# Kernel optimization log

Measured on AMD Instinct MI355X. Metric: run time of the kernel, lower is better.

## Reference

```python
import jax, jax.numpy as jnp
import numpy as np

ALPHA = 0.01  # ema_decay

def setup_inputs() -> dict:
    key = jax.random.key(0)
    k1, k2 = jax.random.split(key)
    B, S, H = 8, 2048, 2048
    x = jax.random.normal(k1, (B, S, H), dtype=jnp.float32)
    W = jax.random.normal(k2, (H, H), dtype=jnp.float32) * (1.0 / np.sqrt(H))
    b = jnp.zeros((H,), dtype=jnp.float32)
    return {"x": x, "W": W, "b": b}

def reference(x, W, b):
    B, S, H = x.shape
    dt = x.dtype
    # p = [S-1, S-2, ..., 0]; w_prime = (1-alpha)^p
    p = jnp.arange(S - 1, -1, -1, dtype=dt)
    one_m_a = jnp.asarray(1.0 - ALPHA, dtype=dt)
    w_prime = one_m_a ** p                                   # [S]
    # w = w_prime, but positions t>=1 scaled by alpha
    w = jnp.where(jnp.arange(S) >= 1, w_prime * ALPHA, w_prime)  # [S]
    c = jnp.cumsum(x * w[None, :, None], axis=1)             # [B,S,H]
    s = c / w_prime[None, :, None]                           # [B,S,H]
    # nn.Linear: s @ W^T + b
    return jnp.einsum('bsh,oh->bso', s, W) + b
```

## Files before the change

### kernel.cpp

```cpp
#include <hip/hip_runtime.h>
#include <cstdint>
#include <cstddef>

#define ALPHA 0.01f
#define A1    0.99f
#define B_    8
#define S_    2048
#define H_    2048
#define NCH   8
#define CL    256
#define NKT   32

typedef __attribute__((ext_vector_type(8))) short bf16x8;
typedef __attribute__((ext_vector_type(4))) float f32x4;

__device__ __forceinline__ unsigned short f2bf(float f) {
    unsigned int u = __float_as_uint(f);
    u += 0x7FFFu + ((u >> 16) & 1u);
    return (unsigned short)(u >> 16);
}

__device__ __forceinline__ void gld16(const void* g, void* l) {
    __builtin_amdgcn_global_load_lds(
        (const __attribute__((address_space(1))) unsigned int*)g,
        (__attribute__((address_space(3))) unsigned int*)l, 16, 0, 0);
}

__global__ void ema_cast_w(const float* __restrict__ W, short* __restrict__ Wb) {
    int i = (blockIdx.x * 256 + threadIdx.x) * 4;
    float4 v = *(const float4*)(W + i);
    short4 o;
    o.x = (short)f2bf(v.x);
    o.y = (short)f2bf(v.y);
    o.z = (short)f2bf(v.z);
    o.w = (short)f2bf(v.w);
    *(short4*)(Wb + i) = o;
}

__global__ __launch_bounds__(256) void ema_carry_kernel(
        const float* __restrict__ x, float* __restrict__ carry) {
    int bid = blockIdx.x;
    int hg = bid & 3;
    int c  = (bid >> 2) & 7;
    int b  = bid >> 5;
    int h0 = (hg << 9) + (threadIdx.x << 1);
    const float2* px = (const float2*)(x + ((size_t)(b * S_) + (size_t)c * CL) * H_ + h0);
    const int STR = H_ / 2;
    float s0, s1;
    int i0;
    if (c == 0) { float2 v = px[0]; s0 = v.x; s1 = v.y; i0 = 1; }
    else        { s0 = 0.f; s1 = 0.f;                   i0 = 0; }
    #pragma unroll 8
    for (int i = i0; i < CL; ++i) {
        float2 v = px[(size_t)i * STR];
        s0 = fmaf(A1, s0, ALPHA * v.x);
        s1 = fmaf(A1, s1, ALPHA * v.y);
    }
    *(float2*)(carry + ((b << 3) + c) * H_ + h0) = (float2){s0, s1};
}

__global__ __launch_bounds__(256) void ema_apply_kernel(
        const float* __restrict__ x, const float* __restrict__ carry,
        unsigned short* __restrict__ sb) {
    int bid = blockIdx.x;
    int hg = bid & 3;
    int c  = (bid >> 2) & 7;
    int b  = bid >> 5;
    int h0 = (hg << 9) + (threadIdx.x << 1);

    float A256 = A1;
    #pragma unroll
    for (int q = 0; q < 8; ++q) A256 *= A256;

    float c0 = 0.f, c1 = 0.f, f = 1.f;
    for (int j = c - 1; j >= 0; --j) {
        float2 cv = *(const float2*)(carry + ((b << 3) + j) * H_ + h0);
        c0 = fmaf(cv.x, f, c0);
        c1 = fmaf(cv.y, f, c1);
        f *= A256;
    }

    size_t base = ((size_t)(b * S_) + (size_t)c * CL) * H_ + h0;
    const float2* px = (const float2*)(x + base);
    unsigned int*  pu = (unsigned int*)(sb + base);
    const int STR = H_ / 2;
    float s0, s1;
    int i0;
    if (c == 0) {
        float2 v = px[0]; s0 = v.x; s1 = v.y;
        pu[0] = (unsigned int)f2bf(s0) | ((unsigned int)f2bf(s1) << 16);
        i0 = 1;
    } else { s0 = c0; s1 = c1; i0 = 0; }
    #pragma unroll 8
    for (int i = i0; i < CL; ++i) {
        float2 v = px[(size_t)i * STR];
        s0 = fmaf(A1, s0, ALPHA * v.x);
        s1 = fmaf(A1, s1, ALPHA * v.y);
        pu[(size_t)i * STR] = (unsigned int)f2bf(s0) | ((unsigned int)f2bf(s1) << 16);
    }
}


#define BAR __builtin_amdgcn_s_barrier()
#define WAIT_LGKM do { asm volatile("s_waitcnt lgkmcnt(0)" ::: "memory"); \
                       __builtin_amdgcn_sched_barrier(0); } while (0)
#define VMW(n) asm volatile("s_waitcnt vmcnt(" #n ")" ::: "memory")

#define STGA(i, kt, buf) gld16(gA[i] + (size_t)(kt) * 128, &ldsA[buf][((i) << 12) + (w << 9)])
#define STGB(i, kt, buf) gld16(gB[i] + (size_t)(kt) * 128, &ldsB[buf][((i) << 12) + (w << 9)])

#define LDA(mh) do { int ra_ = (wm << 1) | (mh);                                   \
    const char* base_ = (const char*)&ldsA[cur][0]                                 \
        + (((((ra_ & 1) << 1) | (ra_ >> 1))) << 13) + laneRow;                     \
    _Pragma("unroll") for (int m_ = 0; m_ < 4; ++m_) {                             \
        Af[m_][0] = *(const bf16x8*)(base_ + (m_ << 11) + ck0);                    \
        Af[m_][1] = *(const bf16x8*)(base_ + (m_ << 11) + ck1); } } while (0)

#define LDB(nh) do { const char* base_ = (const char*)&ldsB[cur][0]                \
        + ((nh) << 14) + (wn << 12) + laneRow;                                     \
    _Pragma("unroll") for (int n_ = 0; n_ < 2; ++n_) {                             \
        Bf[(nh) * 2 + n_][0] = *(const bf16x8*)(base_ + (n_ << 11) + ck0);         \
        Bf[(nh) * 2 + n_][1] = *(const bf16x8*)(base_ + (n_ << 11) + ck1); } } while (0)

#define MM(mh, nh) do { __builtin_amdgcn_s_setprio(1);                             \
    _Pragma("unroll") for (int m_ = 0; m_ < 4; ++m_)                               \
    _Pragma("unroll") for (int n_ = 0; n_ < 2; ++n_)                               \
    _Pragma("unroll") for (int k_ = 0; k_ < 2; ++k_)                               \
        acc[(mh) * 4 + m_][(nh) * 2 + n_] = __builtin_amdgcn_mfma_f32_16x16x32_bf16( \
            Af[m_][k_], Bf[(nh) * 2 + n_][k_], acc[(mh) * 4 + m_][(nh) * 2 + n_], 0, 0, 0); \
    __builtin_amdgcn_s_setprio(0); } while (0)

__global__ __launch_bounds__(512, 2) void ema_gemm_kernel(
        const short* __restrict__ Sb, const short* __restrict__ Wb,
        const float* __restrict__ bias, float* __restrict__ out) {
    __shared__ short ldsA[2][16384];
    __shared__ short ldsB[2][16384];

    int bid = blockIdx.x;
    int swz = ((bid & 7) << 6) | (bid >> 3);
    int tm = swz >> 3;
    int tn = swz & 7;

    int tid  = threadIdx.x;
    int lane = tid & 63;
    int w    = tid >> 6;
    int wm   = w >> 2;
    int wn   = w & 3;

    const int K2 = H_ * 2;
    int rowA = tm << 8;
    int rowB = tn << 8;

    int rowoff = (w << 3) + (lane >> 3);
    int colb   = ((lane & 7) << 4) ^ ((lane >> 5) << 5);
    const char* SbB = (const char*)Sb;
    const char* WbB = (const char*)Wb;
    const char* gA[4];
    const char* gB[4];
    #pragma unroll
    for (int i = 0; i < 4; ++i) {
        int lq = ((i & 1) << 1) | (i >> 1);
        gA[i] = SbB + (size_t)(rowA + lq * 64 + rowoff) * K2 + colb;
        int pos = 2 * i + (w >> 2);
        int ls  = ((pos & 3) << 1) | (pos >> 2);
        gB[i] = WbB + (size_t)(rowB + ls * 32 + ((w & 3) << 3) + (lane >> 3)) * K2 + colb;
    }

    int laneRow = (lane & 15) << 7;
    int ck0 = ((lane >> 4) << 4) ^ (((lane >> 2) & 1) << 5);
    int ck1 = ck0 | 64;

    f32x4 acc[8][4];
    #pragma unroll
    for (int i = 0; i < 8; ++i)
        #pragma unroll
        for (int j = 0; j < 4; ++j)
            acc[i][j] = (f32x4){0.f, 0.f, 0.f, 0.f};
    bf16x8 Af[4][2], Bf[4][2];

    int colg = (tn << 8) + (wn << 6) + (lane & 15);
    float bb[4];
    #pragma unroll
    for (int n = 0; n < 4; ++n) bb[n] = bias[colg + (n << 4)];

    STGA(0, 0, 0); STGA(1, 0, 0); STGB(0, 0, 0); STGB(1, 0, 0);
    STGA(2, 0, 0); STGA(3, 0, 0); STGB(2, 0, 0); STGB(3, 0, 0);
    STGA(0, 1, 1); STGA(1, 1, 1); STGB(0, 1, 1); STGB(1, 1, 1);
    VMW(6);
    BAR;

    for (int t = 0; t < NKT; ++t) {
        int cur = t & 1, nxt = cur ^ 1;
        bool i01 = (t < NKT - 1), i23 = (t < NKT - 2);
        LDA(0); LDB(0);
        if (i01) { STGA(2, t + 1, nxt); STGA(3, t + 1, nxt); }
        BAR; WAIT_LGKM;
        MM(0, 0);
        if (i01) { VMW(6); }
        BAR;
        LDB(1);
        if (i01) { STGB(2, t + 1, nxt); STGB(3, t + 1, nxt); }
        BAR; WAIT_LGKM;
        MM(0, 1);
        BAR;
        LDA(1);
        if (i23) { STGA(0, t + 2, cur); STGA(1, t + 2, cur); }
        BAR; WAIT_LGKM;
        MM(1, 0);
        BAR;
        if (i23) { STGB(0, t + 2, cur); STGB(1, t + 2, cur); }
        BAR;
        MM(1, 1);
        if (t == NKT - 2) { VMW(0); }
        else if (t < NKT - 2) { VMW(6); }
        BAR;
    }

    int rowg = (tm << 8) + (wm << 7) + ((lane >> 4) << 2);
    #pragma unroll
    for (int m = 0; m < 8; ++m) {
        #pragma unroll
        for (int n = 0; n < 4; ++n) {
            int c = colg + (n << 4);
            size_t rb = (size_t)(rowg + (m << 4)) << 11;
            #pragma unroll
            for (int q = 0; q < 4; ++q)
                out[rb + ((size_t)q << 11) + c] = acc[m][n][q] + bb[n];
        }
    }
}

extern "C" void kernel_launch(void* const* d_in, const int* in_sizes, int n_in,
                              void* d_out, int out_size, void* d_ws, size_t ws_size,
                              hipStream_t stream) {
    const float* x    = (const float*)d_in[0];
    const float* W    = (const float*)d_in[1];
    const float* bias = (const float*)d_in[2];
    float* out = (float*)d_out;

    char* ws = (char*)d_ws;
    size_t s_bytes = (size_t)B_ * S_ * H_ * 2;
    size_t w_bytes = (size_t)H_ * H_ * 2;
    unsigned short* s_bf  = (unsigned short*)ws;
    short*          w_bf  = (short*)(ws + s_bytes);
    float*          carry = (float*)(ws + s_bytes + w_bytes);

    ema_cast_w<<<(H_ * H_) / 1024, 256, 0, stream>>>(W, w_bf);
    ema_carry_kernel<<<B_ * NCH * (H_ / 512), 256, 0, stream>>>(x, carry);
    ema_apply_kernel<<<B_ * NCH * (H_ / 512), 256, 0, stream>>>(x, carry, s_bf);
    ema_gemm_kernel<<<(16384 / 256) * (2048 / 256), 512, 0, stream>>>(
        (const short*)s_bf, w_bf, bias, out);
}
```

Baseline: 203.0 us.

## Shrink GEMM tile to 128x256 with BK=32 and raise occupancy to four blocks

Reworks the bf16 GEMM to use 128x256 output tiles with a K step of 32 instead of 256x256 tiles with K step 64. Each step now does one combined LDS fragment load and a single MFMA phase, with simpler double-buffered staging and a new LDS swizzle. It also halves accumulator registers so launch bounds can allow four blocks per CU, aiming to hide latency through occupancy. The cost is less data reuse per tile, twice as many K iterations and barriers, and more global traffic for W.

Measured after the change: 206.3 us. No clear change (+1.6%).

```diff
diff --git a/kernel.cpp b/kernel.cpp
--- a/kernel.cpp
+++ b/kernel.cpp
@@ -9,7 +9,7 @@
 #define H_    2048
 #define NCH   8
 #define CL    256
-#define NKT   32
+#define NKT   64
 
 typedef __attribute__((ext_vector_type(8))) short bf16x8;
 typedef __attribute__((ext_vector_type(4))) float f32x4;
@@ -106,38 +106,32 @@
                        __builtin_amdgcn_sched_barrier(0); } while (0)
 #define VMW(n) asm volatile("s_waitcnt vmcnt(" #n ")" ::: "memory")
 
-#define STGA(i, kt, buf) gld16(gA[i] + (size_t)(kt) * 128, &ldsA[buf][((i) << 12) + (w << 9)])
-#define STGB(i, kt, buf) gld16(gB[i] + (size_t)(kt) * 128, &ldsB[buf][((i) << 12) + (w << 9)])
-
-#define LDA(mh) do { int ra_ = (wm << 1) | (mh);                                   \
-    const char* base_ = (const char*)&ldsA[cur][0]                                 \
-        + (((((ra_ & 1) << 1) | (ra_ >> 1))) << 13) + laneRow;                     \
-    _Pragma("unroll") for (int m_ = 0; m_ < 4; ++m_) {                             \
-        Af[m_][0] = *(const bf16x8*)(base_ + (m_ << 11) + ck0);                    \
-        Af[m_][1] = *(const bf16x8*)(base_ + (m_ << 11) + ck1); } } while (0)
-
-#define LDB(nh) do { const char* base_ = (const char*)&ldsB[cur][0]                \
-        + ((nh) << 14) + (wn << 12) + laneRow;                                     \
-    _Pragma("unroll") for (int n_ = 0; n_ < 2; ++n_) {                             \
-        Bf[(nh) * 2 + n_][0] = *(const bf16x8*)(base_ + (n_ << 11) + ck0);         \
-        Bf[(nh) * 2 + n_][1] = *(const bf16x8*)(base_ + (n_ << 11) + ck1); } } while (0)
-
-#define MM(mh, nh) do { __builtin_amdgcn_s_setprio(1);                             \
-    _Pragma("unroll") for (int m_ = 0; m_ < 4; ++m_)                               \
-    _Pragma("unroll") for (int n_ = 0; n_ < 2; ++n_)                               \
-    _Pragma("unroll") for (int k_ = 0; k_ < 2; ++k_)                               \
-        acc[(mh) * 4 + m_][(nh) * 2 + n_] = __builtin_amdgcn_mfma_f32_16x16x32_bf16( \
-            Af[m_][k_], Bf[(nh) * 2 + n_][k_], acc[(mh) * 4 + m_][(nh) * 2 + n_], 0, 0, 0); \
+#define STGA(kt, buf)    gld16(gA  + (size_t)(kt) * 64, &ldsA[buf][w << 9])
+#define STGB(j, kt, buf) gld16(((j) ? gB1 : gB0) + (size_t)(kt) * 64, \
+                               &ldsB[buf][((j) << 12) + (w << 9)])
+
+#define LDAB do {                                                                  \
+    const char* aB_ = (const char*)&ldsA[cur][0] + (wm << 12) + laneRow + cb;      \
+    const char* bB_ = (const char*)&ldsB[cur][0] + (wn << 12) + laneRow + cb;      \
+    _Pragma("unroll") for (int q_ = 0; q_ < 4; ++q_) {                             \
+        Af[q_] = *(const bf16x8*)(aB_ + (q_ << 10));                               \
+        Bf[q_] = *(const bf16x8*)(bB_ + (q_ << 10)); } } while (0)
+
+#define MM do { __builtin_amdgcn_s_setprio(1);                                     \
+    _Pragma("unroll") for (int mi_ = 0; mi_ < 4; ++mi_)                            \
+    _Pragma("unroll") for (int n_ = 0; n_ < 4; ++n_)                               \
+        acc[mi_][n_] = __builtin_amdgcn_mfma_f32_16x16x32_bf16(                    \
+            Af[mi_], Bf[n_], acc[mi_][n_], 0, 0, 0);                               \
     __builtin_amdgcn_s_setprio(0); } while (0)
 
-__global__ __launch_bounds__(512, 2) void ema_gemm_kernel(
+__global__ __launch_bounds__(512, 4) void ema_gemm_kernel(
         const short* __restrict__ Sb, const short* __restrict__ Wb,
         const float* __restrict__ bias, float* __restrict__ out) {
-    __shared__ short ldsA[2][16384];
-    __shared__ short ldsB[2][16384];
+    __shared__ short ldsA[2][4096];
+    __shared__ short ldsB[2][8192];
 
     int bid = blockIdx.x;
-    int swz = ((bid & 7) << 6) | (bid >> 3);
+    int swz = ((bid & 7) << 7) | (bid >> 3);
     int tm = swz >> 3;
     int tn = swz & 7;
 
@@ -148,84 +142,60 @@
     int wn   = w & 3;
 
     const int K2 = H_ * 2;
-    int rowA = tm << 8;
+    int rowA = tm << 7;
     int rowB = tn << 8;
 
-    int rowoff = (w << 3) + (lane >> 3);
-    int colb   = ((lane & 7) << 4) ^ ((lane >> 5) << 5);
-    const char* SbB = (const char*)Sb;
-    const char* WbB = (const char*)Wb;
-    const char* gA[4];
-    const char* gB[4];
-    #pragma unroll
-    for (int i = 0; i < 4; ++i) {
-        int lq = ((i & 1) << 1) | (i >> 1);
-        gA[i] = SbB + (size_t)(rowA + lq * 64 + rowoff) * K2 + colb;
-        int pos = 2 * i + (w >> 2);
-        int ls  = ((pos & 3) << 1) | (pos >> 2);
-        gB[i] = WbB + (size_t)(rowB + ls * 32 + ((w & 3) << 3) + (lane >> 3)) * K2 + colb;
-    }
-
-    int laneRow = (lane & 15) << 7;
-    int ck0 = ((lane >> 4) << 4) ^ (((lane >> 2) & 1) << 5);
-    int ck1 = ck0 | 64;
-
-    f32x4 acc[8][4];
-    #pragma unroll
-    for (int i = 0; i < 8; ++i)
+    int strow = (w << 4) + (lane >> 2);
+    int colb  = (((lane & 3) ^ ((lane >> 3) & 3)) << 4);
+    const char* gA  = (const char*)Sb + (size_t)(rowA + strow) * K2 + colb;
+    const char* gB0 = (const char*)Wb + (size_t)(rowB + strow) * K2 + colb;
+    const char* gB1 = (const char*)Wb + (size_t)(rowB + 128 + strow) * K2 + colb;
+
+    int laneRow = (lane & 15) << 6;
+    int cb = ((lane >> 4) ^ ((lane >> 1) & 3)) << 4;
+
+    f32x4 acc[4][4];
+    #pragma unroll
+    for (int i = 0; i < 4; ++i)
         #pragma unroll
         for (int j = 0; j < 4; ++j)
             acc[i][j] = (f32x4){0.f, 0.f, 0.f, 0.f};
-    bf16x8 Af[4][2], Bf[4][2];
+    bf16x8 Af[4], Bf[4];
 
     int colg = (tn << 8) + (wn << 6) + (lane & 15);
     float bb[4];
     #pragma unroll
     for (int n = 0; n < 4; ++n) bb[n] = bias[colg + (n << 4)];
 
-    STGA(0, 0, 0); STGA(1, 0, 0); STGB(0, 0, 0); STGB(1, 0, 0);
-    STGA(2, 0, 0); STGA(3, 0, 0); STGB(2, 0, 0); STGB(3, 0, 0);
-    STGA(0, 1, 1); STGA(1, 1, 1); STGB(0, 1, 1); STGB(1, 1, 1);
-    VMW(6);
+    STGA(0, 0); STGB(0, 0, 0); STGB(1, 0, 0);
+    STGA(1, 1); STGB(0, 1, 1); STGB(1, 1, 1);
+    VMW(3);
     BAR;
 
     for (int t = 0; t < NKT; ++t) {
-        int cur = t & 1, nxt = cur ^ 1;
-        bool i01 = (t < NKT - 1), i23 = (t < NKT - 2);
-        LDA(0); LDB(0);
-        if (i01) { STGA(2, t + 1, nxt); STGA(3, t + 1, nxt); }
-        BAR; WAIT_LGKM;
-        MM(0, 0);
-        if (i01) { VMW(6); }
+        int cur = t & 1;
+        LDAB;
         BAR;
-        LDB(1);
-        if (i01) { STGB(2, t + 1, nxt); STGB(3, t + 1, nxt); }
-        BAR; WAIT_LGKM;
-        MM(0, 1);
+        WAIT_LGKM;
+        if (t < NKT - 2) {
+            STGA(t + 2, cur); STGB(0, t + 2, cur); STGB(1, t + 2, cur);
+        }
+        MM;
+        if (t < NKT - 2)       { VMW(3); }
+        else if (t == NKT - 2) { VMW(0); }
         BAR;
-        LDA(1);
-        if (i23) { STGA(0, t + 2, cur); STGA(1, t + 2, cur); }
-        BAR; WAIT_LGKM;
-        MM(1, 0);
-        BAR;
-        if (i23) { STGB(0, t + 2, cur); STGB(1, t + 2, cur); }
-        BAR;
-        MM(1, 1);
-        if (t == NKT - 2) { VMW(0); }
-        else if (t < NKT - 2) { VMW(6); }
-        BAR;
-    }
-
-    int rowg = (tm << 8) + (wm << 7) + ((lane >> 4) << 2);
-    #pragma unroll
-    for (int m = 0; m < 8; ++m) {
+    }
+
+    int rowg = (tm << 7) + (wm << 6) + ((lane >> 4) << 2);
+    #pragma unroll
+    for (int mi = 0; mi < 4; ++mi) {
         #pragma unroll
         for (int n = 0; n < 4; ++n) {
             int c = colg + (n << 4);
-            size_t rb = (size_t)(rowg + (m << 4)) << 11;
+            size_t rb = (size_t)(rowg + (mi << 4)) << 11;
             #pragma unroll
             for (int q = 0; q < 4; ++q)
-                out[rb + ((size_t)q << 11) + c] = acc[m][n][q] + bb[n];
+                out[rb + ((size_t)q << 11) + c] = acc[mi][n][q] + bb[n];
         }
     }
 }
@@ -248,6 +218,6 @@
     ema_cast_w<<<(H_ * H_) / 1024, 256, 0, stream>>>(W, w_bf);
     ema_carry_kernel<<<B_ * NCH * (H_ / 512), 256, 0, stream>>>(x, carry);
     ema_apply_kernel<<<B_ * NCH * (H_ / 512), 256, 0, stream>>>(x, carry, s_bf);
-    ema_gemm_kernel<<<(16384 / 256) * (2048 / 256), 512, 0, stream>>>(
+    ema_gemm_kernel<<<(16384 / 128) * (2048 / 256), 512, 0, stream>>>(
         (const short*)s_bf, w_bf, bias, out);
 }
```
